# Optimization experiments

Measured on AMD Instinct MI355X. Metric: run time of the kernel, lower is better.

Reference implementation:

```python
import jax, jax.numpy as jnp
import numpy as np

IN_FEATURES = 4096
OUT_FEATURES = 4096
RANK = 16
TOKENS = 8192


def setup_inputs() -> dict:
    key = jax.random.key(0)
    k1, k2, k3, k4, k5 = jax.random.split(key, 5)
    x = jax.random.normal(k1, (TOKENS, IN_FEATURES), dtype=jnp.float32)
    orig_weight = jax.random.normal(k2, (IN_FEATURES, OUT_FEATURES), dtype=jnp.float32) * 0.02
    lora_u = jax.random.normal(k3, (IN_FEATURES, RANK), dtype=jnp.float32) * 0.02
    lora_s = jax.random.uniform(k4, (RANK,), dtype=jnp.float32)
    lora_vt = jax.random.normal(k5, (RANK, OUT_FEATURES), dtype=jnp.float32) * 0.02
    return {"x": x, "orig_weight": orig_weight, "lora_u": lora_u,
            "lora_s": lora_s, "lora_vt": lora_vt}


def reference(x, orig_weight, lora_u, lora_s, lora_vt):
    # Faithful to torch: W = orig_weight + lora_u @ diag(lora_s) @ lora_vt; out = x @ W
    # diag(s) contraction expressed as a column scale of lora_u (same math).
    delta = (lora_u * lora_s[None, :]) @ lora_vt  # [in, out] low-rank delta
    return x @ (orig_weight + delta)
```

## Files before the change

### kernel.cpp

```cpp
#include <hip/hip_runtime.h>
#include <hip/hip_bf16.h>
#include <stdint.h>

#define TOKENS 8192
#define NF 4096
#define KF 4096
#define RANK 16

typedef __attribute__((ext_vector_type(8))) short bf16x8;
typedef __attribute__((ext_vector_type(4))) float f32x4;
typedef __attribute__((ext_vector_type(8))) unsigned short u16x8;

static __device__ __forceinline__ unsigned short f2b(float f) {
    union { float f; uint32_t u; } v; v.f = f;
    uint32_t u = v.u;
    uint32_t r = (u + 0x7fffu + ((u >> 16) & 1u)) >> 16;
    return (unsigned short)r;
}

__global__ __launch_bounds__(256) void prep_w_kernel(
    const float* __restrict__ W, const float* __restrict__ U,
    const float* __restrict__ s, const float* __restrict__ Vt,
    unsigned short* __restrict__ Wt)
{
    __shared__ float Us[64][16];
    __shared__ float Vs[16][64];
    __shared__ float tile[64][65];
    const int kb = blockIdx.x, nb = blockIdx.y;
    const int t = threadIdx.x;
    for (int idx = t; idx < 64 * 16; idx += 256) {
        int kl = idx >> 4, r = idx & 15;
        Us[kl][r] = U[(size_t)(kb * 64 + kl) * RANK + r];
    }
    for (int idx = t; idx < 16 * 64; idx += 256) {
        int r = idx >> 6, nl = idx & 63;
        Vs[r][nl] = Vt[(size_t)r * NF + nb * 64 + nl] * s[r];
    }
    __syncthreads();
    const int nl = t & 63, kl0 = t >> 6;
    for (int i = 0; i < 16; ++i) {
        int kl = kl0 + i * 4;
        float v = W[(size_t)(kb * 64 + kl) * NF + nb * 64 + nl];
        #pragma unroll
        for (int r = 0; r < RANK; ++r) v += Us[kl][r] * Vs[r][nl];
        tile[kl][nl] = v;
    }
    __syncthreads();
    const int klw = t & 63, nl0 = t >> 6;
    for (int i = 0; i < 16; ++i) {
        int nlw = nl0 + i * 4;
        Wt[(size_t)(nb * 64 + nlw) * KF + kb * 64 + klw] = f2b(tile[klw][nlw]);
    }
}

__global__ __launch_bounds__(256) void prep_x_kernel(
    const float* __restrict__ x, unsigned short* __restrict__ xb)
{
    size_t base = ((size_t)blockIdx.x * 256 + threadIdx.x) * 8;
    float4 a = *(const float4*)(x + base);
    float4 b = *(const float4*)(x + base + 4);
    u16x8 o;
    o[0] = f2b(a.x); o[1] = f2b(a.y); o[2] = f2b(a.z); o[3] = f2b(a.w);
    o[4] = f2b(b.x); o[5] = f2b(b.y); o[6] = f2b(b.z); o[7] = f2b(b.w);
    *(u16x8*)(xb + base) = o;
}


#define VM4  asm volatile("s_waitcnt vmcnt(4)" ::: "memory")
#define NOVM

#define PHASE(d, q, bfr, STAGE_STMT, VMW) do {                                  \
    bf16x8 af0k0 = ldA(d, 2*(q), 0),   af0k1 = ldA(d, 2*(q), 1);                \
    bf16x8 af1k0 = ldA(d, 2*(q)+1, 0), af1k1 = ldA(d, 2*(q)+1, 1);              \
    STAGE_STMT;                                                                 \
    VMW;                                                                        \
    __builtin_amdgcn_s_barrier();                                               \
    asm volatile("s_waitcnt lgkmcnt(0)" ::: "memory");                          \
    __builtin_amdgcn_s_setprio(1);                                              \
    _Pragma("unroll")                                                           \
    for (int nf = 0; nf < 4; ++nf) {                                            \
        acc[2*(q)][nf]   = __builtin_amdgcn_mfma_f32_16x16x32_bf16(af0k0, bfr[nf][0], acc[2*(q)][nf],   0,0,0); \
        acc[2*(q)][nf]   = __builtin_amdgcn_mfma_f32_16x16x32_bf16(af0k1, bfr[nf][1], acc[2*(q)][nf],   0,0,0); \
        acc[2*(q)+1][nf] = __builtin_amdgcn_mfma_f32_16x16x32_bf16(af1k0, bfr[nf][0], acc[2*(q)+1][nf], 0,0,0); \
        acc[2*(q)+1][nf] = __builtin_amdgcn_mfma_f32_16x16x32_bf16(af1k1, bfr[nf][1], acc[2*(q)+1][nf], 0,0,0); \
    }                                                                           \
    __builtin_amdgcn_s_setprio(0);                                              \
    __builtin_amdgcn_s_barrier();                                               \
} while (0)

#define LDB_ALL(d, bfr) do {                                                    \
    _Pragma("unroll")                                                           \
    for (int nf = 0; nf < 4; ++nf) {                                            \
        bfr[nf][0] = ldB(d, nf, 0);                                             \
        bfr[nf][1] = ldB(d, nf, 1);                                             \
    } } while (0)

__global__ __launch_bounds__(512, 2) void gemm_kernel(
    const unsigned short* __restrict__ A,
    const unsigned short* __restrict__ Bt,
    float* __restrict__ C)
{
    __shared__ __align__(16) unsigned short lds[65536];

    const int tid  = threadIdx.x;
    const int lane = tid & 63;
    const int wave = tid >> 6;
    const int wm = wave >> 2;
    const int wn = wave & 3;

    const int bid = blockIdx.x;
    const int swz = (bid & 7) * 64 + (bid >> 3);
    const int tm = swz >> 4;
    const int tn = swz & 15;

    const int frow = lane & 15;
    const int kgrp = lane >> 4;
    const int xorv = (frow & 7) << 4;

    const int st_row  = tid >> 3;
    const int st_colE = ((((tid & 7) * 16) ^ (((tid >> 3) & 7) << 4)) >> 1);
    const unsigned short* aSrc = A  + (size_t)(tm * 256 + st_row) * KF + st_colE;
    const unsigned short* bSrc = Bt + (size_t)(tn * 256 + st_row) * KF + st_colE;
    const int dstE = tid * 8;

    f32x4 acc[8][4] = {};

    auto stage = [&](int isB, int d, int h, int kt) {
        const unsigned short* src =
            (isB ? bSrc : aSrc) + (size_t)((h) * 128) * KF + (kt) * 64;
        unsigned short* dst = (unsigned short*)&lds[isB * 32768 + (d * 2 + h) * 8192 + dstE];
        __builtin_amdgcn_global_load_lds(
            (const __attribute__((address_space(1))) void*)src,
            (__attribute__((address_space(3))) void*)dst, 16, 0, 0);
        __builtin_amdgcn_global_load_lds(
            (const __attribute__((address_space(1))) void*)(src + (size_t)64 * KF),
            (__attribute__((address_space(3))) void*)(dst + 4096), 16, 0, 0);
    };

    auto ldA = [&](int d, int mf, int kk) -> bf16x8 {
        int off = (d * 2 + wm) * 8192 + (mf * 16 + frow) * 64
                + ((((kk << 6) | (kgrp << 4)) ^ xorv) >> 1);
        return *(const bf16x8*)&lds[off];
    };
    auto ldB = [&](int d, int nf, int kk) -> bf16x8 {
        int off = 32768 + (d * 2 + (wn >> 1)) * 8192
                + ((wn & 1) * 64 + nf * 16 + frow) * 64
                + ((((kk << 6) | (kgrp << 4)) ^ xorv) >> 1);
        return *(const bf16x8*)&lds[off];
    };

    stage(1, 0, 0, 0); stage(1, 0, 1, 0);
    stage(0, 0, 0, 0); stage(0, 0, 1, 0);
    stage(1, 1, 0, 1); stage(1, 1, 1, 1);
    VM4;
    __builtin_amdgcn_s_barrier();

    for (int i = 0; i < 32; ++i) {
        const int kt1 = 2 * i + 1;
        const int kt2 = (2 * i + 2) & 63;
        const int kt3 = (2 * i + 3) & 63;

        bf16x8 bfr[4][2];
        LDB_ALL(0, bfr);
        PHASE(0, 0, bfr, stage(0, 1, 0, kt1), NOVM);
        PHASE(0, 1, bfr, stage(0, 1, 1, kt1), NOVM);
        PHASE(0, 2, bfr, stage(1, 0, 0, kt2), NOVM);
        PHASE(0, 3, bfr, stage(1, 0, 1, kt2), VM4);
        LDB_ALL(1, bfr);
        PHASE(1, 0, bfr, stage(0, 0, 0, kt2), NOVM);
        PHASE(1, 1, bfr, stage(0, 0, 1, kt2), NOVM);
        PHASE(1, 2, bfr, stage(1, 1, 0, kt3), NOVM);
        PHASE(1, 3, bfr, stage(1, 1, 1, kt3), VM4);
    }

    asm volatile("s_waitcnt vmcnt(0)" ::: "memory");

    const int rgrp = lane >> 4, coll = lane & 15;
    #pragma unroll
    for (int mf = 0; mf < 8; ++mf)
        #pragma unroll
        for (int nf = 0; nf < 4; ++nf) {
            size_t row0 = (size_t)(tm * 256 + wm * 128 + mf * 16 + rgrp * 4);
            size_t col  = (size_t)(tn * 256 + wn * 64 + nf * 16 + coll);
            #pragma unroll
            for (int r = 0; r < 4; ++r)
                C[(row0 + r) * NF + col] = acc[mf][nf][r];
        }
}

extern "C" void kernel_launch(void* const* d_in, const int* in_sizes, int n_in,
                              void* d_out, int out_size, void* d_ws, size_t ws_size,
                              hipStream_t stream) {
    const float* x  = (const float*)d_in[0];
    const float* W  = (const float*)d_in[1];
    const float* U  = (const float*)d_in[2];
    const float* s  = (const float*)d_in[3];
    const float* Vt = (const float*)d_in[4];
    float* out = (float*)d_out;

    unsigned short* Wt = (unsigned short*)d_ws;
    unsigned short* xb = Wt + (size_t)NF * KF;

    prep_w_kernel<<<dim3(KF / 64, NF / 64), 256, 0, stream>>>(W, U, s, Vt, Wt);
    prep_x_kernel<<<(TOKENS * KF / 8) / 256, 256, 0, stream>>>(x, xb);
    gemm_kernel<<<(TOKENS / 256) * (NF / 256), 512, 0, stream>>>(xb, Wt, out);
}
```

Before: 299.3 us.

## Vectorize Wt transpose stores, add nontemporal hints, front-load GEMM staging

```diff
diff --git a/kernel.cpp b/kernel.cpp
--- a/kernel.cpp
+++ b/kernel.cpp
@@ -40,16 +40,20 @@
     const int nl = t & 63, kl0 = t >> 6;
     for (int i = 0; i < 16; ++i) {
         int kl = kl0 + i * 4;
-        float v = W[(size_t)(kb * 64 + kl) * NF + nb * 64 + nl];
+        float v = __builtin_nontemporal_load(&W[(size_t)(kb * 64 + kl) * NF + nb * 64 + nl]);
         #pragma unroll
         for (int r = 0; r < RANK; ++r) v += Us[kl][r] * Vs[r][nl];
         tile[kl][nl] = v;
     }
     __syncthreads();
-    const int klw = t & 63, nl0 = t >> 6;
-    for (int i = 0; i < 16; ++i) {
-        int nlw = nl0 + i * 4;
-        Wt[(size_t)(nb * 64 + nlw) * KF + kb * 64 + klw] = f2b(tile[klw][nlw]);
+    #pragma unroll
+    for (int j = 0; j < 2; ++j) {
+        int idx = t + j * 256;
+        int kg = idx & 7, n = idx >> 3;
+        u16x8 o;
+        #pragma unroll
+        for (int e = 0; e < 8; ++e) o[e] = f2b(tile[kg * 8 + e][n]);
+        *(u16x8*)&Wt[(size_t)(nb * 64 + n) * KF + kb * 64 + kg * 8] = o;
     }
 }
 
@@ -57,11 +61,11 @@
     const float* __restrict__ x, unsigned short* __restrict__ xb)
 {
     size_t base = ((size_t)blockIdx.x * 256 + threadIdx.x) * 8;
-    float4 a = *(const float4*)(x + base);
-    float4 b = *(const float4*)(x + base + 4);
+    f32x4 a = __builtin_nontemporal_load((const f32x4*)(x + base));
+    f32x4 b = __builtin_nontemporal_load((const f32x4*)(x + base + 4));
     u16x8 o;
-    o[0] = f2b(a.x); o[1] = f2b(a.y); o[2] = f2b(a.z); o[3] = f2b(a.w);
-    o[4] = f2b(b.x); o[5] = f2b(b.y); o[6] = f2b(b.z); o[7] = f2b(b.w);
+    o[0] = f2b(a[0]); o[1] = f2b(a[1]); o[2] = f2b(a[2]); o[3] = f2b(a[3]);
+    o[4] = f2b(b[0]); o[5] = f2b(b[1]); o[6] = f2b(b[2]); o[7] = f2b(b[3]);
     *(u16x8*)(xb + base) = o;
 }
 
@@ -69,10 +73,10 @@
 #define VM4  asm volatile("s_waitcnt vmcnt(4)" ::: "memory")
 #define NOVM
 
-#define PHASE(d, q, bfr, STAGE_STMT, VMW) do {                                  \
+#define PHASE(d, q, bfr, STAGE_EXPR, VMW) do {                                  \
     bf16x8 af0k0 = ldA(d, 2*(q), 0),   af0k1 = ldA(d, 2*(q), 1);                \
     bf16x8 af1k0 = ldA(d, 2*(q)+1, 0), af1k1 = ldA(d, 2*(q)+1, 1);              \
-    STAGE_STMT;                                                                 \
+    STAGE_EXPR;                                                                 \
     VMW;                                                                        \
     __builtin_amdgcn_s_barrier();                                               \
     asm volatile("s_waitcnt lgkmcnt(0)" ::: "memory");                          \
@@ -162,15 +166,15 @@
 
         bf16x8 bfr[4][2];
         LDB_ALL(0, bfr);
-        PHASE(0, 0, bfr, stage(0, 1, 0, kt1), NOVM);
-        PHASE(0, 1, bfr, stage(0, 1, 1, kt1), NOVM);
-        PHASE(0, 2, bfr, stage(1, 0, 0, kt2), NOVM);
-        PHASE(0, 3, bfr, stage(1, 0, 1, kt2), VM4);
+        PHASE(0, 0, bfr, (stage(0, 1, 0, kt1), stage(0, 1, 1, kt1)), NOVM);
+        PHASE(0, 1, bfr, stage(1, 0, 0, kt2), NOVM);
+        PHASE(0, 2, bfr, stage(1, 0, 1, kt2), NOVM);
+        PHASE(0, 3, bfr, (void)0, VM4);
         LDB_ALL(1, bfr);
         PHASE(1, 0, bfr, stage(0, 0, 0, kt2), NOVM);
-        PHASE(1, 1, bfr, stage(0, 0, 1, kt2), NOVM);
-        PHASE(1, 2, bfr, stage(1, 1, 0, kt3), NOVM);
-        PHASE(1, 3, bfr, stage(1, 1, 1, kt3), VM4);
+        PHASE(1, 1, bfr, (stage(0, 0, 1, kt2), stage(1, 1, 0, kt3)), NOVM);
+        PHASE(1, 2, bfr, stage(1, 1, 1, kt3), NOVM);
+        PHASE(1, 3, bfr, (void)0, VM4);
     }
 
     asm volatile("s_waitcnt vmcnt(0)" ::: "memory");
@@ -184,7 +188,7 @@
             size_t col  = (size_t)(tn * 256 + wn * 64 + nf * 16 + coll);
             #pragma unroll
             for (int r = 0; r < 4; ++r)
-                C[(row0 + r) * NF + col] = acc[mf][nf][r];
+                __builtin_nontemporal_store(acc[mf][nf][r], &C[(row0 + r) * NF + col]);
         }
 }
 
```

New measurement: 305.3 us. 2.0% more time.
